# Performance work log

Measured on AMD Instinct MI355X. Metric: run time of the kernel, lower is better.

Reference implementation:

```python
import jax, jax.numpy as jnp
import numpy as np

B, L1, L2, H = 8, 384, 384, 128


def _lin(k, out_f, in_f, scale=0.05):
    kw, kb = jax.random.split(k)
    return (jax.random.normal(kw, (out_f, in_f), jnp.float32) * scale,
            jax.random.normal(kb, (out_f,), jnp.float32) * scale)


def setup_inputs() -> dict:
    key = jax.random.key(0)
    ks = jax.random.split(key, 10)
    Wq_w, Wq_b = _lin(ks[2], H, H)
    Wup_w, Wup_b = _lin(ks[3], H, H)
    Wvp_w, Wvp_b = _lin(ks[4], H, H)
    V_w, V_b = _lin(ks[5], 1, H)
    Wg_w, Wg_b = _lin(ks[6], 2 * H, 2 * H)
    W_ih, b_ih = _lin(ks[7], 4 * H, 2 * H)
    W_hh, b_hh = _lin(ks[8], 4 * H, H)
    return {
        "x": jax.random.normal(ks[0], (B, L1, H), jnp.float32),
        "x_mask": jnp.zeros((B, L1), dtype=bool),
        "y": jax.random.normal(ks[1], (B, L2, H), jnp.float32),
        "y_mask": jnp.zeros((B, L2), dtype=bool),
        "Wq_w": Wq_w, "Wq_b": Wq_b,
        "Wup_w": Wup_w, "Wup_b": Wup_b,
        "Wvp_w": Wvp_w, "Wvp_b": Wvp_b,
        "V_w": V_w, "V_b": V_b,
        "Wg_w": Wg_w, "Wg_b": Wg_b,
        "W_ih": W_ih, "W_hh": W_hh, "b_ih": b_ih, "b_hh": b_hh,
    }


def reference(x, x_mask, y, y_mask, Wq_w, Wq_b, Wup_w, Wup_b, Wvp_w, Wvp_b,
              V_w, V_b, Wg_w, Wg_b, W_ih, W_hh, b_ih, b_hh):
    b, l1, h = x.shape
    # projections (torch Linear: x @ W.T + b)
    x_proj = x @ Wup_w.T + Wup_b                      # [B, L1, H]
    y_proj = y @ Wq_w.T + Wq_b                        # [B, L2, H]
    # source feeds a constant zero hidden state into W_vp -> just its bias
    hidden_proj = jnp.zeros((h,), x.dtype) @ Wvp_w.T + Wvp_b  # [H]
    # additive attention scores: V . tanh(xp + yp + hp)
    sum_batch = jnp.tanh(x_proj[:, :, None, :] + y_proj[:, None, :, :] + hidden_proj)  # [B,L1,L2,H]
    s = jnp.einsum('btjh,h->btj', sum_batch, V_w[0]) + V_b[0]  # [B, L1, L2]
    # sum_mask = (1 - x_mask) outer (1 - y_mask)
    xm = 1.0 - x_mask.astype(s.dtype)
    ym = 1.0 - y_mask.astype(s.dtype)
    s = s * (xm[:, :, None] * ym[:, None, :])
    s = jnp.where(y_mask[:, None, :], -jnp.inf, s)
    alpha = jax.nn.softmax(s, axis=-1)                # [B, L1, L2]
    ct = jnp.einsum('btj,bjh->bth', alpha, y)         # [B, L1, H]
    merge = jnp.concatenate([x, ct], axis=2)          # [B, L1, 2H]
    gt = jax.nn.sigmoid(merge @ Wg_w.T + Wg_b)
    lstm_in = gt * merge                              # [B, L1, 2H]
    # single-layer unidirectional LSTM (torch gate order: i, f, g, o)
    gates_x = lstm_in @ W_ih.T + b_ih                 # [B, L1, 4H]

    def step(carry, gx):
        h_t, c_t = carry
        g = gx + h_t @ W_hh.T + b_hh
        i, f, gg, o = jnp.split(g, 4, axis=-1)
        c_n = jax.nn.sigmoid(f) * c_t + jax.nn.sigmoid(i) * jnp.tanh(gg)
        h_n = jax.nn.sigmoid(o) * jnp.tanh(c_n)
        return (h_n, c_n), h_n

    init = (jnp.zeros((b, h), x.dtype), jnp.zeros((b, h), x.dtype))
    _, hs = jax.lax.scan(step, init, jnp.swapaxes(gates_x, 0, 1))  # [L1, B, H]
    return jnp.swapaxes(hs, 0, 1)                     # [B, L1, H]
```

## Files before the change

### kernel.cpp

```cpp
#include <hip/hip_runtime.h>
#include <hip/hip_bf16.h>
#include <math.h>

typedef __attribute__((ext_vector_type(4))) float  float4v;
typedef __attribute__((ext_vector_type(2))) float  float2v;
typedef __attribute__((ext_vector_type(8))) short  short8;

#define B_ 8
#define L_ 384
#define H_ 128

__device__ __forceinline__ float bflo(unsigned int u){ unsigned int t = u << 16; float f; __builtin_memcpy(&f,&t,4); return f; }
__device__ __forceinline__ unsigned short f2bf(float f){
  unsigned int t; __builtin_memcpy(&t,&f,4);
  return (unsigned short)((t + 0x7fffu + ((t>>16)&1u)) >> 16);
}
__device__ __forceinline__ float fsig(float x){ return __fdividef(1.f, 1.f + __expf(-x)); }

__device__ __forceinline__ void barrier_lds(){
  asm volatile("s_waitcnt lgkmcnt(0)\n\ts_barrier" ::: "memory");
}

template<int K>
__device__ __forceinline__ void mfma_rowgemm_body(
    unsigned short* in_s,
    const float* __restrict__ inA,
    const float* __restrict__ W, const float* __restrict__ bias,
    const float* __restrict__ bias2, float* __restrict__ out,
    int Ntotal, int act, int row0, int ob)
{
  constexpr int KP = K + 2;
  const int tid  = threadIdx.x;
  const int w    = tid >> 6;
  const int l    = tid & 63;
  const int c    = l & 15;
  const int quad = l >> 4;

  #pragma unroll
  for (int it = 0; it < K/32; ++it) {
    int idx = it*256 + tid;
    int r = idx / (K/4);
    int k = (idx % (K/4)) * 4;
    float4v f = *(const float4v*)(inA + (size_t)(row0+r)*K + k);
    unsigned int p0 = (unsigned int)f2bf(f.x) | ((unsigned int)f2bf(f.y) << 16);
    unsigned int p1 = (unsigned int)f2bf(f.z) | ((unsigned int)f2bf(f.w) << 16);
    *(unsigned int*)&in_s[r*KP + k]     = p0;
    *(unsigned int*)&in_s[r*KP + k + 2] = p1;
  }

  const int n = ob + w*16 + c;
  short8 bfr[K/32];
  #pragma unroll
  for (int kt = 0; kt < K/32; ++kt) {
    const float* src = W + (size_t)n*K + kt*32 + quad*8;
    float4v f0 = *(const float4v*)(src);
    float4v f1 = *(const float4v*)(src + 4);
    short8 v;
    v[0]=(short)f2bf(f0[0]); v[1]=(short)f2bf(f0[1]); v[2]=(short)f2bf(f0[2]); v[3]=(short)f2bf(f0[3]);
    v[4]=(short)f2bf(f1[0]); v[5]=(short)f2bf(f1[1]); v[6]=(short)f2bf(f1[2]); v[7]=(short)f2bf(f1[3]);
    bfr[kt] = v;
  }
  __syncthreads();

  const float4v z4 = {0.f,0.f,0.f,0.f};
  float4v acc0 = z4, acc1 = z4;
  #pragma unroll
  for (int kt = 0; kt < K/32; ++kt) {
    short8 a0 = *(const short8*)&in_s[(c     )*KP + kt*32 + quad*8];
    short8 a1 = *(const short8*)&in_s[(16 + c)*KP + kt*32 + quad*8];
    acc0 = __builtin_amdgcn_mfma_f32_16x16x32_bf16(a0, bfr[kt], acc0, 0,0,0);
    acc1 = __builtin_amdgcn_mfma_f32_16x16x32_bf16(a1, bfr[kt], acc1, 0,0,0);
  }

  const float C2 = 2.8853900817779268f;
  float bv = bias[n] + (bias2 ? bias2[n] : 0.f);
  #pragma unroll
  for (int mt = 0; mt < 2; ++mt) {
    float4v A = mt ? acc1 : acc0;
    #pragma unroll
    for (int r = 0; r < 4; ++r) {
      int m = mt*16 + quad*4 + r;
      float val = A[r] + bv;
      if (act == 4)
        val = __builtin_amdgcn_exp2f(C2 * val);
      if (act == 3)
        out[(size_t)(row0+m)*Ntotal + (n & 127)*4 + (n >> 7)] = val;
      else
        out[(size_t)(row0+m)*Ntotal + n] = val;
    }
  }
}

template<int K>
__global__ __launch_bounds__(256) void mfma_rowgemm_kernel(
    const float* __restrict__ inA,
    const float* __restrict__ W, const float* __restrict__ bias,
    const float* __restrict__ bias2, float* __restrict__ out,
    int Ntotal, int act)
{
  __shared__ __align__(16) unsigned short in_s[32*(K+2)];
  mfma_rowgemm_body<K>(in_s, inA, W, bias, bias2, out,
                       Ntotal, act, blockIdx.x*32, blockIdx.y*64);
}

__global__ __launch_bounds__(256) void proj_mfma_kernel(
    const float* __restrict__ x, const float* __restrict__ y,
    const float* __restrict__ Wup_w, const float* __restrict__ Wup_b,
    const float* __restrict__ Wq_w, const float* __restrict__ Wq_b,
    const float* __restrict__ Wvp_b,
    float* __restrict__ xp, float* __restrict__ yp)
{
  __shared__ __align__(16) unsigned short in_s[32*130];
  int bx = blockIdx.x;
  if (bx < 192)
    mfma_rowgemm_body<128>(in_s, x, Wup_w, Wup_b, nullptr,
                           xp, 128, 4, (bx>>1)*32, (bx&1)*64);
  else {
    bx -= 192;
    mfma_rowgemm_body<128>(in_s, y, Wq_w, Wq_b, Wvp_b,
                           yp, 128, 4, (bx>>1)*32, (bx&1)*64);
  }
}

__global__ __launch_bounds__(256) void attn_kernel(
    const float* __restrict__ xp, const float* __restrict__ yp,
    const float* __restrict__ y, const unsigned char* __restrict__ xmask,
    const unsigned char* __restrict__ ymask, const float* __restrict__ Vw,
    const float* __restrict__ Vb,
    float* __restrict__ ctpbase, float* __restrict__ ml)
{
  __shared__ __align__(16) float xp_s[8][128];
  __shared__ __align__(16) float v2_s[128];
  __shared__ __align__(16) float yp_s[32][132];
  __shared__ __align__(16) unsigned short p_s[16][40];
  __shared__ float sc_s[16];
  __shared__ float xm_s[8];
  __shared__ float ym_s[32];
  __shared__ float sv_s;
  const int tid = threadIdx.x;
  const int b   = blockIdx.y;
  const int t0  = blockIdx.x * 8;
  const int jh  = blockIdx.z;
  const int jb  = jh * 96;
  const int w    = tid >> 6;
  const int l    = tid & 63;
  const int c16  = l & 15;
  const int quad = l >> 4;
  {
    int r = tid >> 5, k4 = (tid & 31) * 4;
    float4v f = *(const float4v*)(xp + ((size_t)(b*L_ + t0 + r))*H_ + k4);
    *(float4v*)&xp_s[r][k4] = f;
    if (tid < 32) {
      float4v v = *(const float4v*)(Vw + tid*4);
      float4v v2; v2[0]=2.f*v[0]; v2[1]=2.f*v[1]; v2[2]=2.f*v[2]; v2[3]=2.f*v[3];
      *(float4v*)&v2_s[tid*4] = v2;
    }
    if (tid < 8) xm_s[tid] = xmask[b*L_ + t0 + tid] ? 0.f : 1.f;
    if (tid < 16) sc_s[tid] = 0.f;
    for (int i = 320 + tid; i < 640; i += 256) ((unsigned short*)p_s)[i] = 0;
  }
  __syncthreads();
  if (tid < 32) {
    float4v v = *(const float4v*)&v2_s[tid*4];
    float sm = (v[0]+v[1]) + (v[2]+v[3]);
    #pragma unroll
    for (int off = 16; off >= 1; off >>= 1) sm += __shfl_xor(sm, off);
    if (tid == 0) sv_s = 0.5f*sm + Vb[0];
  }

  float4v rp[4];
  unsigned char ymb = 0;
  {
    #pragma unroll
    for (int it = 0; it < 4; ++it) {
      int idx = it*256 + tid; int r = idx >> 5; int k4 = (idx & 31) * 4;
      rp[it] = *(const float4v*)(yp + ((size_t)(b*L_ + jb + r))*H_ + k4);
    }
    if (tid < 32) ymb = ymask[b*L_ + jb + tid];
  }

  const int t = tid >> 5, u = tid & 31;
  float mrun = -__builtin_inff(), lrun = 0.f;
  const float4v z4 = {0.f,0.f,0.f,0.f};
  float4v acc0 = z4, acc1 = z4;
  float svc = 0.f, xmv = 0.f;

  for (int c = 0; c < 3; ++c) {
    __syncthreads();
    #pragma unroll
    for (int it = 0; it < 4; ++it) {
      int idx = it*256 + tid; int r = idx >> 5; int k4 = (idx & 31) * 4;
      *(float4v*)&yp_s[r][k4] = rp[it];
    }
    if (tid < 32) ym_s[tid] = ymb ? 0.f : 1.f;
    __syncthreads();
    if (c == 0) { svc = sv_s; xmv = xm_s[t]; }
    short8 yb0, yb1;
    {
      const float* ybase = y + ((size_t)(b*L_ + jb + c*32 + quad*8))*H_ + c16;
      #pragma unroll
      for (int jj = 0; jj < 8; ++jj) {
        yb0[jj] = (short)f2bf(ybase[(size_t)jj*H_ + w*16]);
        yb1[jj] = (short)f2bf(ybase[(size_t)jj*H_ + (w+4)*16]);
      }
    }
    if (c < 2) {
      #pragma unroll
      for (int it = 0; it < 4; ++it) {
        int idx = it*256 + tid; int r = idx >> 5; int k4 = (idx & 31) * 4;
        rp[it] = *(const float4v*)(yp + ((size_t)(b*L_ + jb + (c+1)*32 + r))*H_ + k4);
      }
      if (tid < 32) ymb = ymask[b*L_ + jb + (c+1)*32 + tid];
    }

    float sA = 0.f, sB = 0.f;
    {
      const float* yr = yp_s[u];
      const float* xr = xp_s[t];
      #pragma unroll 4
      for (int k = 0; k < 128; k += 4) {
        float4v yv = *(const float4v*)&yr[k];
        float4v xv = *(const float4v*)&xr[k];
        float4v vv = *(const float4v*)&v2_s[k];
        sA -= vv[0] * __builtin_amdgcn_rcpf(__builtin_fmaf(xv[0], yv[0], 1.f));
        sB -= vv[1] * __builtin_amdgcn_rcpf(__builtin_fmaf(xv[1], yv[1], 1.f));
        sA -= vv[2] * __builtin_amdgcn_rcpf(__builtin_fmaf(xv[2], yv[2], 1.f));
        sB -= vv[3] * __builtin_amdgcn_rcpf(__builtin_fmaf(xv[3], yv[3], 1.f));
      }
    }
    float ymv = ym_s[u];
    float s = (svc + sA + sB) * xmv * ymv;
    if (ymv == 0.f) s = -__builtin_inff();
    float mc = s;
    #pragma unroll
    for (int off = 16; off >= 1; off >>= 1) mc = fmaxf(mc, __shfl_xor(mc, off));
    float mnew = fmaxf(mrun, mc);
    float p  = __expf(s - mnew);
    float sc = __expf(mrun - mnew);
    float ps = p;
    #pragma unroll
    for (int off = 16; off >= 1; off >>= 1) ps += __shfl_xor(ps, off);
    lrun = lrun * sc + ps;
    mrun = mnew;
    p_s[t][u] = f2bf(p);
    if (u == 0) sc_s[t] = sc;
    __syncthreads();
    short8 pf = *(const short8*)&p_s[c16][quad*8];
    float4v scv;
    #pragma unroll
    for (int r = 0; r < 4; ++r) scv[r] = sc_s[quad*4 + r];
    acc0 *= scv; acc1 *= scv;
    acc0 = __builtin_amdgcn_mfma_f32_16x16x32_bf16(pf, yb0, acc0, 0,0,0);
    acc1 = __builtin_amdgcn_mfma_f32_16x16x32_bf16(pf, yb1, acc1, 0,0,0);
  }
  float* ctp = ctpbase + (size_t)jh*393216;
  if (quad < 2) {
    #pragma unroll
    for (int r = 0; r < 4; ++r) {
      int row = b*L_ + t0 + quad*4 + r;
      ctp[(size_t)row*H_ + w*16 + c16]     = acc0[r];
      ctp[(size_t)row*H_ + (w+4)*16 + c16] = acc1[r];
    }
  }
  if (u == 0) {
    int row = b*L_ + t0 + t;
    ml[(jh*2+0)*3072 + row] = mrun;
    ml[(jh*2+1)*3072 + row] = lrun;
  }
}

__global__ __launch_bounds__(256) void gate1_kernel(
    const float* __restrict__ x,
    const float* __restrict__ ctpbase, const float* __restrict__ ml,
    const float* __restrict__ Wg_w, const float* __restrict__ Wg_b,
    float* __restrict__ out)
{
  constexpr int K = 256, KP = 258;
  __shared__ __align__(16) unsigned short in_s[32*KP];
  const int tid  = threadIdx.x;
  const int w    = tid >> 6;
  const int l    = tid & 63;
  const int c    = l & 15;
  const int quad = l >> 4;
  const int row0 = blockIdx.x * 32;
  const int ob   = blockIdx.y * 64;

  #pragma unroll
  for (int it = 0; it < 8; ++it) {
    int idx = it*256 + tid;
    int r = idx >> 6;
    int k = (idx & 63) * 4;
    int row = row0 + r;
    float4v f;
    if (k < 128) {
      f = *(const float4v*)(x + (size_t)row*128 + k);
    } else {
      float m0 = ml[       row], l0 = ml[  3072 + row];
      float m1 = ml[2*3072+row], l1 = ml[3*3072 + row];
      float m2 = ml[4*3072+row], l2 = ml[5*3072 + row];
      float m3 = ml[6*3072+row], l3 = ml[7*3072 + row];
      float mm = fmaxf(fmaxf(m0, m1), fmaxf(m2, m3));
      float e0 = __expf(m0-mm), e1 = __expf(m1-mm);
      float e2 = __expf(m2-mm), e3 = __expf(m3-mm);
      float inv = __fdividef(1.f, (l0*e0 + l1*e1) + (l2*e2 + l3*e3));
      size_t off = (size_t)row*128 + (k-128);
      float4v v0 = *(const float4v*)(ctpbase             + off);
      float4v v1 = *(const float4v*)(ctpbase +   393216  + off);
      float4v v2 = *(const float4v*)(ctpbase + 2*393216  + off);
      float4v v3 = *(const float4v*)(ctpbase + 3*393216  + off);
      f[0] = ((v0[0]*e0 + v1[0]*e1) + (v2[0]*e2 + v3[0]*e3))*inv;
      f[1] = ((v0[1]*e0 + v1[1]*e1) + (v2[1]*e2 + v3[1]*e3))*inv;
      f[2] = ((v0[2]*e0 + v1[2]*e1) + (v2[2]*e2 + v3[2]*e3))*inv;
      f[3] = ((v0[3]*e0 + v1[3]*e1) + (v2[3]*e2 + v3[3]*e3))*inv;
    }
    unsigned int p0 = (unsigned int)f2bf(f[0]) | ((unsigned int)f2bf(f[1]) << 16);
    unsigned int p1 = (unsigned int)f2bf(f[2]) | ((unsigned int)f2bf(f[3]) << 16);
    *(unsigned int*)&in_s[r*KP + k]     = p0;
    *(unsigned int*)&in_s[r*KP + k + 2] = p1;
  }

  const int n = ob + w*16 + c;
  short8 bfr[8];
  #pragma unroll
  for (int kt = 0; kt < 8; ++kt) {
    const float* src = Wg_w + (size_t)n*K + kt*32 + quad*8;
    float4v f0 = *(const float4v*)(src);
    float4v f1 = *(const float4v*)(src + 4);
    short8 v;
    v[0]=(short)f2bf(f0[0]); v[1]=(short)f2bf(f0[1]); v[2]=(short)f2bf(f0[2]); v[3]=(short)f2bf(f0[3]);
    v[4]=(short)f2bf(f1[0]); v[5]=(short)f2bf(f1[1]); v[6]=(short)f2bf(f1[2]); v[7]=(short)f2bf(f1[3]);
    bfr[kt] = v;
  }
  __syncthreads();

  const float4v z4 = {0.f,0.f,0.f,0.f};
  float4v acc0 = z4, acc1 = z4;
  #pragma unroll
  for (int kt = 0; kt < 8; ++kt) {
    short8 a0 = *(const short8*)&in_s[(c     )*KP + kt*32 + quad*8];
    short8 a1 = *(const short8*)&in_s[(16 + c)*KP + kt*32 + quad*8];
    acc0 = __builtin_amdgcn_mfma_f32_16x16x32_bf16(a0, bfr[kt], acc0, 0,0,0);
    acc1 = __builtin_amdgcn_mfma_f32_16x16x32_bf16(a1, bfr[kt], acc1, 0,0,0);
  }

  float bv = Wg_b[n];
  #pragma unroll
  for (int mt = 0; mt < 2; ++mt) {
    float4v A = mt ? acc1 : acc0;
    #pragma unroll
    for (int r = 0; r < 4; ++r) {
      int m = mt*16 + quad*4 + r;
      float val = A[r] + bv;
      float mg = bflo((unsigned int)in_s[m*KP + n]);
      out[(size_t)(row0+m)*256 + n] = fsig(val) * mg;
    }
  }
}

__global__ __launch_bounds__(512) void lstm_kernel(
    const float* __restrict__ gx, const float* __restrict__ Whh,
    float* __restrict__ out)
{
  __shared__ __align__(16) unsigned short h_s[2][128];
  const int tid  = threadIdx.x;
  const int b    = blockIdx.x;
  const int w    = tid >> 6;
  const int l    = tid & 63;
  const int col  = l & 15;
  const int quad = l >> 4;

  short8 bf[4][4];
  #pragma unroll
  for (int nt = 0; nt < 4; ++nt) {
    const int n = nt*128 + w*16 + col;
    #pragma unroll
    for (int kt = 0; kt < 4; ++kt) {
      const int k0 = kt*32 + quad*8;
      const float* src = Whh + (size_t)n*H_ + k0;
      float4v f0 = *(const float4v*)(src);
      float4v f1 = *(const float4v*)(src + 4);
      short8 v;
      v[0]=(short)f2bf(f0[0]); v[1]=(short)f2bf(f0[1]); v[2]=(short)f2bf(f0[2]); v[3]=(short)f2bf(f0[3]);
      v[4]=(short)f2bf(f1[0]); v[5]=(short)f2bf(f1[1]); v[6]=(short)f2bf(f1[2]); v[7]=(short)f2bf(f1[3]);
      bf[nt][kt] = v;
    }
  }

  if (tid < 128) { h_s[0][tid] = 0; h_s[1][tid] = 0; }
  float cst = 0.f;
  const int goff = w*16 + col;
  const float* gbase = gx + (size_t)b*L_*512 + goff*4;
  float* outp = out + (size_t)b*L_*H_ + goff;
  float4v gbuf[4];
  #pragma unroll
  for (int s = 0; s < 4; ++s)
    gbuf[s] = *(const float4v*)(gbase + (size_t)s*512);
  const float4v z4 = {0.f,0.f,0.f,0.f};
  const float NL2E = -1.4426950408889634f;
  const float P2L2E = 2.8853900817779268f;
  __syncthreads();

  for (int t4 = 0; t4 < L_; t4 += 4) {
    #pragma unroll
    for (int s = 0; s < 4; ++s) {
      const int tstep = t4 + s;
      const unsigned short* hb = h_s[s & 1];
      short8 a0 = *(const short8*)&hb[ 0 + quad*8];
      short8 a1 = *(const short8*)&hb[32 + quad*8];
      short8 a2 = *(const short8*)&hb[64 + quad*8];
      short8 a3 = *(const short8*)&hb[96 + quad*8];
      float4v gcur = gbuf[s];
      if (tstep + 4 < L_)
        gbuf[s] = *(const float4v*)(gbase + (size_t)(tstep+4)*512);
      float4v c2a = __builtin_amdgcn_mfma_f32_16x16x32_bf16(a0, bf[2][0], z4, 0,0,0);
      float4v c0a = __builtin_amdgcn_mfma_f32_16x16x32_bf16(a0, bf[0][0], z4, 0,0,0);
      float4v c2b = __builtin_amdgcn_mfma_f32_16x16x32_bf16(a1, bf[2][1], z4, 0,0,0);
      float4v c0b = __builtin_amdgcn_mfma_f32_16x16x32_bf16(a1, bf[0][1], z4, 0,0,0);
      c2a = __builtin_amdgcn_mfma_f32_16x16x32_bf16(a2, bf[2][2], c2a, 0,0,0);
      c0a = __builtin_amdgcn_mfma_f32_16x16x32_bf16(a2, bf[0][2], c0a, 0,0,0);
      c2b = __builtin_amdgcn_mfma_f32_16x16x32_bf16(a3, bf[2][3], c2b, 0,0,0);
      c0b = __builtin_amdgcn_mfma_f32_16x16x32_bf16(a3, bf[0][3], c0b, 0,0,0);
      float4v c1a = __builtin_amdgcn_mfma_f32_16x16x32_bf16(a0, bf[1][0], z4, 0,0,0);
      float4v c3a = __builtin_amdgcn_mfma_f32_16x16x32_bf16(a0, bf[3][0], z4, 0,0,0);
      float4v c1b = __builtin_amdgcn_mfma_f32_16x16x32_bf16(a1, bf[1][1], z4, 0,0,0);
      float4v c3b = __builtin_amdgcn_mfma_f32_16x16x32_bf16(a1, bf[3][1], z4, 0,0,0);
      float gg = 1.f - 2.f*__builtin_amdgcn_rcpf(
                   __builtin_amdgcn_exp2f(P2L2E*((c2a[0]+c2b[0]) + gcur[2])) + 1.f);
      float ig = __builtin_amdgcn_rcpf(
                   1.f + __builtin_amdgcn_exp2f(NL2E*((c0a[0]+c0b[0]) + gcur[0])));
      c1a = __builtin_amdgcn_mfma_f32_16x16x32_bf16(a2, bf[1][2], c1a, 0,0,0);
      c3a = __builtin_amdgcn_mfma_f32_16x16x32_bf16(a2, bf[3][2], c3a, 0,0,0);
      float igg = ig * gg;
      c1b = __builtin_amdgcn_mfma_f32_16x16x32_bf16(a3, bf[1][3], c1b, 0,0,0);
      c3b = __builtin_amdgcn_mfma_f32_16x16x32_bf16(a3, bf[3][3], c3b, 0,0,0);
      float fg = __builtin_amdgcn_rcpf(
                   1.f + __builtin_amdgcn_exp2f(NL2E*((c1a[0]+c1b[0]) + gcur[1])));
      float og = __builtin_amdgcn_rcpf(
                   1.f + __builtin_amdgcn_exp2f(NL2E*((c3a[0]+c3b[0]) + gcur[3])));
      cst = fg*cst + igg;
      float hn = og * (1.f - 2.f*__builtin_amdgcn_rcpf(
                   __builtin_amdgcn_exp2f(P2L2E*cst) + 1.f));
      if (quad == 0) {
        outp[(size_t)tstep*H_] = hn;
        h_s[(s+1)&1][goff] = f2bf(hn);
      }
      barrier_lds();
    }
  }
}

extern "C" void kernel_launch(void* const* d_in, const int* in_sizes, int n_in,
                              void* d_out, int out_size, void* d_ws, size_t ws_size,
                              hipStream_t stream)
{
  (void)in_sizes; (void)n_in; (void)out_size; (void)ws_size;
  const float* x     = (const float*)d_in[0];
  const unsigned char* xm = (const unsigned char*)d_in[1];
  const float* y     = (const float*)d_in[2];
  const unsigned char* ym = (const unsigned char*)d_in[3];
  const float* Wq_w  = (const float*)d_in[4];
  const float* Wq_b  = (const float*)d_in[5];
  const float* Wup_w = (const float*)d_in[6];
  const float* Wup_b = (const float*)d_in[7];
  const float* Wvp_b = (const float*)d_in[9];
  const float* V_w   = (const float*)d_in[10];
  const float* V_b   = (const float*)d_in[11];
  const float* Wg_w  = (const float*)d_in[12];
  const float* Wg_b  = (const float*)d_in[13];
  const float* W_ih  = (const float*)d_in[14];
  const float* W_hh  = (const float*)d_in[15];
  const float* b_ih  = (const float*)d_in[16];
  const float* b_hh  = (const float*)d_in[17];
  float* out = (float*)d_out;

  float* wsf    = (float*)d_ws;
  float* xp_ws  = wsf;
  float* yp_ws  = xp_ws + 393216;
  float* li_ws  = xp_ws;
  float* ctp_ws = yp_ws + 393216;
  float* gx_ws  = ctp_ws + 4*393216;
  float* ml_ws  = gx_ws + 1572864;

  proj_mfma_kernel<<<dim3(384),256,0,stream>>>(x, y, Wup_w, Wup_b, Wq_w, Wq_b, Wvp_b, xp_ws, yp_ws);
  attn_kernel<<<dim3(48,8,4),256,0,stream>>>(xp_ws, yp_ws, y, xm, ym, V_w, V_b, ctp_ws, ml_ws);
  gate1_kernel<<<dim3(96,4),256,0,stream>>>(x, ctp_ws, ml_ws, Wg_w, Wg_b, li_ws);
  mfma_rowgemm_kernel<256><<<dim3(96,8),256,0,stream>>>(li_ws, W_ih, b_ih, b_hh, gx_ws, 512, 3);
  lstm_kernel<<<dim3(8),512,0,stream>>>(gx_ws, W_hh, out);
}
```

Measured before the change: 330.1 us.

## Process multiple output-column tiles per block to reuse staged input rows

Each GEMM block (projection, gate, input-to-gate) now loops over several 64-column output tiles and reuses the bf16 input rows already staged in shared memory. This cuts the number of blocks and the repeated load and convert of the activation rows. The weight fragments for the next tile are loaded into a second register buffer while the current tile's MFMAs run. The price is fewer blocks, which lowers parallelism on a large GPU, and higher register pressure from the double-buffered weights.

```diff
diff --git a/kernel.cpp b/kernel.cpp
--- a/kernel.cpp
+++ b/kernel.cpp
@@ -21,13 +21,13 @@
   asm volatile("s_waitcnt lgkmcnt(0)\n\ts_barrier" ::: "memory");
 }
 
-template<int K>
+template<int K, int NOB>
 __device__ __forceinline__ void mfma_rowgemm_body(
     unsigned short* in_s,
     const float* __restrict__ inA,
     const float* __restrict__ W, const float* __restrict__ bias,
     const float* __restrict__ bias2, float* __restrict__ out,
-    int Ntotal, int act, int row0, int ob)
+    int Ntotal, int act, int row0, int ob0)
 {
   constexpr int KP = K + 2;
   const int tid  = threadIdx.x;
@@ -48,50 +48,72 @@
     *(unsigned int*)&in_s[r*KP + k + 2] = p1;
   }
 
-  const int n = ob + w*16 + c;
-  short8 bfr[K/32];
+  short8 bfr[2][K/32];
+  {
+    const int n0 = ob0 + w*16 + c;
+    #pragma unroll
+    for (int kt = 0; kt < K/32; ++kt) {
+      const float* src = W + (size_t)n0*K + kt*32 + quad*8;
+      float4v f0 = *(const float4v*)(src);
+      float4v f1 = *(const float4v*)(src + 4);
+      short8 v;
+      v[0]=(short)f2bf(f0[0]); v[1]=(short)f2bf(f0[1]); v[2]=(short)f2bf(f0[2]); v[3]=(short)f2bf(f0[3]);
+      v[4]=(short)f2bf(f1[0]); v[5]=(short)f2bf(f1[1]); v[6]=(short)f2bf(f1[2]); v[7]=(short)f2bf(f1[3]);
+      bfr[0][kt] = v;
+    }
+  }
+  __syncthreads();
+
+  const float C2 = 2.8853900817779268f;
+  const float4v z4 = {0.f,0.f,0.f,0.f};
+
   #pragma unroll
-  for (int kt = 0; kt < K/32; ++kt) {
-    const float* src = W + (size_t)n*K + kt*32 + quad*8;
-    float4v f0 = *(const float4v*)(src);
-    float4v f1 = *(const float4v*)(src + 4);
-    short8 v;
-    v[0]=(short)f2bf(f0[0]); v[1]=(short)f2bf(f0[1]); v[2]=(short)f2bf(f0[2]); v[3]=(short)f2bf(f0[3]);
-    v[4]=(short)f2bf(f1[0]); v[5]=(short)f2bf(f1[1]); v[6]=(short)f2bf(f1[2]); v[7]=(short)f2bf(f1[3]);
-    bfr[kt] = v;
-  }
-  __syncthreads();
-
-  const float4v z4 = {0.f,0.f,0.f,0.f};
-  float4v acc0 = z4, acc1 = z4;
-  #pragma unroll
-  for (int kt = 0; kt < K/32; ++kt) {
-    short8 a0 = *(const short8*)&in_s[(c     )*KP + kt*32 + quad*8];
-    short8 a1 = *(const short8*)&in_s[(16 + c)*KP + kt*32 + quad*8];
-    acc0 = __builtin_amdgcn_mfma_f32_16x16x32_bf16(a0, bfr[kt], acc0, 0,0,0);
-    acc1 = __builtin_amdgcn_mfma_f32_16x16x32_bf16(a1, bfr[kt], acc1, 0,0,0);
-  }
-
-  const float C2 = 2.8853900817779268f;
-  float bv = bias[n] + (bias2 ? bias2[n] : 0.f);
-  #pragma unroll
-  for (int mt = 0; mt < 2; ++mt) {
-    float4v A = mt ? acc1 : acc0;
-    #pragma unroll
-    for (int r = 0; r < 4; ++r) {
-      int m = mt*16 + quad*4 + r;
-      float val = A[r] + bv;
-      if (act == 4)
-        val = __builtin_amdgcn_exp2f(C2 * val);
-      if (act == 3)
-        out[(size_t)(row0+m)*Ntotal + (n & 127)*4 + (n >> 7)] = val;
-      else
-        out[(size_t)(row0+m)*Ntotal + n] = val;
-    }
-  }
-}
-
-template<int K>
+  for (int obi = 0; obi < NOB; ++obi) {
+    const int cur = obi & 1;
+    const int n = ob0 + obi*64 + w*16 + c;
+    if (obi + 1 < NOB) {
+      const int nn = ob0 + (obi+1)*64 + w*16 + c;
+      #pragma unroll
+      for (int kt = 0; kt < K/32; ++kt) {
+        const float* src = W + (size_t)nn*K + kt*32 + quad*8;
+        float4v f0 = *(const float4v*)(src);
+        float4v f1 = *(const float4v*)(src + 4);
+        short8 v;
+        v[0]=(short)f2bf(f0[0]); v[1]=(short)f2bf(f0[1]); v[2]=(short)f2bf(f0[2]); v[3]=(short)f2bf(f0[3]);
+        v[4]=(short)f2bf(f1[0]); v[5]=(short)f2bf(f1[1]); v[6]=(short)f2bf(f1[2]); v[7]=(short)f2bf(f1[3]);
+        bfr[cur^1][kt] = v;
+      }
+    }
+
+    float4v acc0 = z4, acc1 = z4;
+    #pragma unroll
+    for (int kt = 0; kt < K/32; ++kt) {
+      short8 a0 = *(const short8*)&in_s[(c     )*KP + kt*32 + quad*8];
+      short8 a1 = *(const short8*)&in_s[(16 + c)*KP + kt*32 + quad*8];
+      acc0 = __builtin_amdgcn_mfma_f32_16x16x32_bf16(a0, bfr[cur][kt], acc0, 0,0,0);
+      acc1 = __builtin_amdgcn_mfma_f32_16x16x32_bf16(a1, bfr[cur][kt], acc1, 0,0,0);
+    }
+
+    float bv = bias[n] + (bias2 ? bias2[n] : 0.f);
+    #pragma unroll
+    for (int mt = 0; mt < 2; ++mt) {
+      float4v A = mt ? acc1 : acc0;
+      #pragma unroll
+      for (int r = 0; r < 4; ++r) {
+        int m = mt*16 + quad*4 + r;
+        float val = A[r] + bv;
+        if (act == 4)
+          val = __builtin_amdgcn_exp2f(C2 * val);
+        if (act == 3)
+          out[(size_t)(row0+m)*Ntotal + (n & 127)*4 + (n >> 7)] = val;
+        else
+          out[(size_t)(row0+m)*Ntotal + n] = val;
+      }
+    }
+  }
+}
+
+template<int K, int NOB>
 __global__ __launch_bounds__(256) void mfma_rowgemm_kernel(
     const float* __restrict__ inA,
     const float* __restrict__ W, const float* __restrict__ bias,
@@ -99,8 +121,8 @@
     int Ntotal, int act)
 {
   __shared__ __align__(16) unsigned short in_s[32*(K+2)];
-  mfma_rowgemm_body<K>(in_s, inA, W, bias, bias2, out,
-                       Ntotal, act, blockIdx.x*32, blockIdx.y*64);
+  mfma_rowgemm_body<K, NOB>(in_s, inA, W, bias, bias2, out,
+                            Ntotal, act, blockIdx.x*32, blockIdx.y*64*NOB);
 }
 
 __global__ __launch_bounds__(256) void proj_mfma_kernel(
@@ -112,13 +134,13 @@
 {
   __shared__ __align__(16) unsigned short in_s[32*130];
   int bx = blockIdx.x;
-  if (bx < 192)
-    mfma_rowgemm_body<128>(in_s, x, Wup_w, Wup_b, nullptr,
-                           xp, 128, 4, (bx>>1)*32, (bx&1)*64);
+  if (bx < 96)
+    mfma_rowgemm_body<128, 2>(in_s, x, Wup_w, Wup_b, nullptr,
+                              xp, 128, 4, bx*32, 0);
   else {
-    bx -= 192;
-    mfma_rowgemm_body<128>(in_s, y, Wq_w, Wq_b, Wvp_b,
-                           yp, 128, 4, (bx>>1)*32, (bx&1)*64);
+    bx -= 96;
+    mfma_rowgemm_body<128, 2>(in_s, y, Wq_w, Wq_b, Wvp_b,
+                              yp, 128, 4, bx*32, 0);
   }
 }
 
@@ -283,7 +305,7 @@
   const int c    = l & 15;
   const int quad = l >> 4;
   const int row0 = blockIdx.x * 32;
-  const int ob   = blockIdx.y * 64;
+  const int ob0  = blockIdx.y * 128;
 
   #pragma unroll
   for (int it = 0; it < 8; ++it) {
@@ -319,40 +341,61 @@
     *(unsigned int*)&in_s[r*KP + k + 2] = p1;
   }
 
-  const int n = ob + w*16 + c;
-  short8 bfr[8];
+  short8 bfr[2][8];
+  {
+    const int n0 = ob0 + w*16 + c;
+    #pragma unroll
+    for (int kt = 0; kt < 8; ++kt) {
+      const float* src = Wg_w + (size_t)n0*K + kt*32 + quad*8;
+      float4v f0 = *(const float4v*)(src);
+      float4v f1 = *(const float4v*)(src + 4);
+      short8 v;
+      v[0]=(short)f2bf(f0[0]); v[1]=(short)f2bf(f0[1]); v[2]=(short)f2bf(f0[2]); v[3]=(short)f2bf(f0[3]);
+      v[4]=(short)f2bf(f1[0]); v[5]=(short)f2bf(f1[1]); v[6]=(short)f2bf(f1[2]); v[7]=(short)f2bf(f1[3]);
+      bfr[0][kt] = v;
+    }
+  }
+  __syncthreads();
+
+  const float4v z4 = {0.f,0.f,0.f,0.f};
   #pragma unroll
-  for (int kt = 0; kt < 8; ++kt) {
-    const float* src = Wg_w + (size_t)n*K + kt*32 + quad*8;
-    float4v f0 = *(const float4v*)(src);
-    float4v f1 = *(const float4v*)(src + 4);
-    short8 v;
-    v[0]=(short)f2bf(f0[0]); v[1]=(short)f2bf(f0[1]); v[2]=(short)f2bf(f0[2]); v[3]=(short)f2bf(f0[3]);
-    v[4]=(short)f2bf(f1[0]); v[5]=(short)f2bf(f1[1]); v[6]=(short)f2bf(f1[2]); v[7]=(short)f2bf(f1[3]);
-    bfr[kt] = v;
-  }
-  __syncthreads();
-
-  const float4v z4 = {0.f,0.f,0.f,0.f};
-  float4v acc0 = z4, acc1 = z4;
-  #pragma unroll
-  for (int kt = 0; kt < 8; ++kt) {
-    short8 a0 = *(const short8*)&in_s[(c     )*KP + kt*32 + quad*8];
-    short8 a1 = *(const short8*)&in_s[(16 + c)*KP + kt*32 + quad*8];
-    acc0 = __builtin_amdgcn_mfma_f32_16x16x32_bf16(a0, bfr[kt], acc0, 0,0,0);
-    acc1 = __builtin_amdgcn_mfma_f32_16x16x32_bf16(a1, bfr[kt], acc1, 0,0,0);
-  }
-
-  float bv = Wg_b[n];
-  #pragma unroll
-  for (int mt = 0; mt < 2; ++mt) {
-    float4v A = mt ? acc1 : acc0;
-    #pragma unroll
-    for (int r = 0; r < 4; ++r) {
-      int m = mt*16 + quad*4 + r;
-      float val = A[r] + bv;
-      float mg = bflo((unsigned int)in_s[m*KP + n]);
-      out[(size_t)(row0+m)*256 + n] = fsig(val) * mg;
+  for (int obi = 0; obi < 2; ++obi) {
+    const int cur = obi & 1;
+    const int n = ob0 + obi*64 + w*16 + c;
+    if (obi == 0) {
+      const int nn = ob0 + 64 + w*16 + c;
+      #pragma unroll
+      for (int kt = 0; kt < 8; ++kt) {
+        const float* src = Wg_w + (size_t)nn*K + kt*32 + quad*8;
+        float4v f0 = *(const float4v*)(src);
+        float4v f1 = *(const float4v*)(src + 4);
+        short8 v;
+        v[0]=(short)f2bf(f0[0]); v[1]=(short)f2bf(f0[1]); v[2]=(short)f2bf(f0[2]); v[3]=(short)f2bf(f0[3]);
+        v[4]=(short)f2bf(f1[0]); v[5]=(short)f2bf(f1[1]); v[6]=(short)f2bf(f1[2]); v[7]=(short)f2bf(f1[3]);
+        bfr[1][kt] = v;
+      }
+    }
+
+    float4v acc0 = z4, acc1 = z4;
+    #pragma unroll
+    for (int kt = 0; kt < 8; ++kt) {
+      short8 a0 = *(const short8*)&in_s[(c     )*KP + kt*32 + quad*8];
+      short8 a1 = *(const short8*)&in_s[(16 + c)*KP + kt*32 + quad*8];
+      acc0 = __builtin_amdgcn_mfma_f32_16x16x32_bf16(a0, bfr[cur][kt], acc0, 0,0,0);
+      acc1 = __builtin_amdgcn_mfma_f32_16x16x32_bf16(a1, bfr[cur][kt], acc1, 0,0,0);
+    }
+
+    float bv = Wg_b[n];
+    #pragma unroll
+    for (int mt = 0; mt < 2; ++mt) {
+      float4v A = mt ? acc1 : acc0;
+      #pragma unroll
+      for (int r = 0; r < 4; ++r) {
+        int m = mt*16 + quad*4 + r;
+        float val = A[r] + bv;
+        float mg = bflo((unsigned int)in_s[m*KP + n]);
+        out[(size_t)(row0+m)*256 + n] = fsig(val) * mg;
+      }
     }
   }
 }
@@ -481,9 +524,9 @@
   float* gx_ws  = ctp_ws + 4*393216;
   float* ml_ws  = gx_ws + 1572864;
 
-  proj_mfma_kernel<<<dim3(384),256,0,stream>>>(x, y, Wup_w, Wup_b, Wq_w, Wq_b, Wvp_b, xp_ws, yp_ws);
+  proj_mfma_kernel<<<dim3(192),256,0,stream>>>(x, y, Wup_w, Wup_b, Wq_w, Wq_b, Wvp_b, xp_ws, yp_ws);
   attn_kernel<<<dim3(48,8,4),256,0,stream>>>(xp_ws, yp_ws, y, xm, ym, V_w, V_b, ctp_ws, ml_ws);
-  gate1_kernel<<<dim3(96,4),256,0,stream>>>(x, ctp_ws, ml_ws, Wg_w, Wg_b, li_ws);
-  mfma_rowgemm_kernel<256><<<dim3(96,8),256,0,stream>>>(li_ws, W_ih, b_ih, b_hh, gx_ws, 512, 3);
+  gate1_kernel<<<dim3(96,2),256,0,stream>>>(x, ctp_ws, ml_ws, Wg_w, Wg_b, li_ws);
+  mfma_rowgemm_kernel<256,4><<<dim3(96,2),256,0,stream>>>(li_ws, W_ih, b_ih, b_hh, gx_ws, 512, 3);
   lstm_kernel<<<dim3(8),512,0,stream>>>(gx_ws, W_hh, out);
 }
```

New measurement: 336.8 us. +2.0%, slower.
